# Optimization experiments

Measured on AMD Instinct MI355X. Metric: run time of the kernel, lower is better.

Reference implementation:

```python
import jax, jax.numpy as jnp
import numpy as np

HEADS, DIM_HEAD, LANDMARKS, PINV_ITERS, CONV_K = 8, 64, 256, 6, 33


def iter_pinv(x, iters=PINV_ITERS):
    # Moore-Penrose iterative pseudo-inverse (lucidrains nystrom_attention)
    abs_x = jnp.abs(x)
    scale = abs_x.sum(-1).max() * abs_x.sum(-2).max()  # global maxes, as in torch.max
    z = jnp.swapaxes(x, -1, -2) / scale
    I = jnp.eye(x.shape[-1], dtype=x.dtype)
    for _ in range(iters):
        xz = x @ z
        z = 0.25 * z @ (13.0 * I - xz @ (15.0 * I - xz @ (7.0 * I - xz)))
    return z


def nystrom_attention(h, W_qkv, W_out, b_out, conv_w):
    b, n, _ = h.shape
    inner = HEADS * DIM_HEAD
    qkv = h @ W_qkv  # (b, n, 3*inner), bias=False
    q, k, v = jnp.split(qkv, 3, axis=-1)
    split_heads = lambda t: t.reshape(b, n, HEADS, DIM_HEAD).transpose(0, 2, 1, 3)
    q, k, v = split_heads(q), split_heads(k), split_heads(v)  # (b,h,n,dh)
    q = q * (DIM_HEAD ** -0.5)
    l = n // LANDMARKS  # tokens per landmark (n divisible by m, so no padding)
    q_l = q.reshape(b, HEADS, LANDMARKS, l, DIM_HEAD).mean(3)
    k_l = k.reshape(b, HEADS, LANDMARKS, l, DIM_HEAD).mean(3)
    sim1 = jnp.einsum('bhnd,bhmd->bhnm', q, k_l)      # (b,h,n,m)
    sim2 = jnp.einsum('bhmd,bhld->bhml', q_l, k_l)    # (b,h,m,m)
    sim3 = jnp.einsum('bhmd,bhnd->bhmn', q_l, k)      # (b,h,m,n)
    attn1 = jax.nn.softmax(sim1, -1)
    attn2 = jax.nn.softmax(sim2, -1)
    attn3 = jax.nn.softmax(sim3, -1)
    out = (attn1 @ iter_pinv(attn2)) @ (attn3 @ v)    # (b,h,n,dh)
    # residual depthwise conv along sequence dim: Conv2d(heads, heads, (33,1), groups=heads, no bias)
    res = jax.lax.conv_general_dilated(
        v, conv_w, window_strides=(1, 1),
        padding=((CONV_K // 2, CONV_K // 2), (0, 0)),
        feature_group_count=HEADS)
    out = out + res
    out = out.transpose(0, 2, 1, 3).reshape(b, n, inner)
    return out @ W_out + b_out


def setup_inputs() -> dict:
    key = jax.random.key(0)
    ks = jax.random.split(key, 8)
    N, Din, Dout = 8192, 1024, 256
    inner = HEADS * DIM_HEAD
    s = 0.02
    return {
        'x': jax.random.normal(ks[0], (1, N, Din), jnp.float32),
        'W_ft': jax.random.normal(ks[1], (Din, Dout), jnp.float32) * s,
        'b_ft': jnp.zeros((Dout,), jnp.float32),
        'W_qkv': jax.random.normal(ks[2], (Dout, 3 * inner), jnp.float32) * s,
        'W_out': jax.random.normal(ks[3], (inner, Dout), jnp.float32) * s,
        'b_out': jnp.zeros((Dout,), jnp.float32),
        'conv_w': jax.random.normal(ks[4], (HEADS, 1, CONV_K, 1), jnp.float32) * s,
        'W_score': jax.random.normal(ks[5], (Dout, 1), jnp.float32) * s,
        'b_score': jnp.zeros((1,), jnp.float32),
    }


def reference(x, W_ft, b_ft, W_qkv, W_out, b_out, conv_w, W_score, b_score):
    # feature_transform: Linear -> Dropout (identity in eval) -> ReLU
    h = jax.nn.relu(x @ W_ft + b_ft)                 # (1, N, Dout)
    af = nystrom_attention(h, W_qkv, W_out, b_out, conv_w)
    # score_layer: Linear -> Dropout -> ReLU
    scores = jax.nn.relu(af @ W_score + b_score)     # (1, N, 1)
    scores = scores[0].T                             # (1, N)
    weights = jax.nn.softmax(scores, axis=1)         # (1, N)
    aggregated = weights @ h[0]                      # (1, Dout)
    return aggregated, weights
```

## Files before the change

kernel.cpp:

```cpp
#include <hip/hip_runtime.h>

typedef unsigned short u16;
typedef __attribute__((ext_vector_type(8))) short s16x8;
typedef __attribute__((ext_vector_type(4))) float f32x4;
typedef __attribute__((ext_vector_type(8))) unsigned short u16x8;

__device__ inline float b2f(u16 u) {
  unsigned x = ((unsigned)u) << 16;
  return __builtin_bit_cast(float, x);
}
__device__ inline u16 f2b(float f) {
  unsigned u = __builtin_bit_cast(unsigned, f);
  u += 0x7fffu + ((u >> 16) & 1u);
  return (u16)(u >> 16);
}

#define GLL(src, dst) __builtin_amdgcn_global_load_lds( \
    (const __attribute__((address_space(1))) unsigned int*)(src), \
    (__attribute__((address_space(3))) unsigned int*)(dst), 16, 0, 0)

struct MP {
  const u16* A; const u16* B;
  u16* C; u16* Ct; float* Cf; u16* vTo;
  const u16* Aadd; const float* bias;
  int M, N, K;
  int lda, ldb, ldc, ldct, ldcf, ldaadd;
  long long bA, bB, bC, bCt, bCf, bAadd;
  float alpha, beta;
  int relu, scale_cols; float colscale;
  int kchunks;
};

template<int BM, int BN, bool F32A>
__global__ __launch_bounds__(256) void gemm_mfma(MP p)
{
  constexpr int WM = BM / 2, WN = BN / 2;
  constexpr int FM = WM / 16, FN = WN / 16;
  constexpr int APAN = BM / 16, BPAN = BN / 16, NPAN = APAN + BPAN;
  constexpr int APW = (APAN + 3) / 4;
  __shared__ __align__(16) u16 lds[2 * NPAN * 512];

  const int tid = threadIdx.x, lane = tid & 63, wid = tid >> 6;
  const int bz = blockIdx.z;
  const int batch = (p.kchunks > 1) ? bz / p.kchunks : bz;
  const int kc    = (p.kchunks > 1) ? bz % p.kchunks : 0;
  const u16* A = p.A + (long long)batch * p.bA + (long long)kc * p.K;
  const float* Af32 = (const float*)p.A + (long long)batch * p.bA + (long long)kc * p.K;
  const u16* B = p.B + (long long)batch * p.bB + (long long)kc * p.K;
  const int m0 = blockIdx.y * BM, n0 = blockIdx.x * BN;
  const int srow = lane & 15, skoff = (lane >> 4) * 8;
  const int wm0 = (wid >> 1) * WM, wn0 = (wid & 1) * WN;

  f32x4 acc[FM][FN];
#pragma unroll
  for (int i = 0; i < FM; i++)
#pragma unroll
    for (int j = 0; j < FN; j++) acc[i][j] = (f32x4){0.f, 0.f, 0.f, 0.f};

  float4 areg[APW][2];

  auto stage_all = [&](int sb, int kt) {
#pragma unroll
    for (int pp = wid; pp < NPAN; pp += 4) {
      const u16* src = (pp < APAN)
        ? A + (size_t)(m0 + pp * 16 + srow) * p.lda + kt + skoff
        : B + (size_t)(n0 + (pp - APAN) * 16 + srow) * p.ldb + kt + skoff;
      GLL(src, &lds[sb * (NPAN * 512) + pp * 512]);
    }
  };
  auto stage_b = [&](int sb, int kt) {
#pragma unroll
    for (int pp = APAN + wid; pp < NPAN; pp += 4) {
      const u16* src = B + (size_t)(n0 + (pp - APAN) * 16 + srow) * p.ldb + kt + skoff;
      GLL(src, &lds[sb * (NPAN * 512) + pp * 512]);
    }
  };
  auto load_a = [&](int kt) {
#pragma unroll
    for (int ap = 0; ap < APW; ap++) {
      int pp = wid + ap * 4;
      const float* src = Af32 + (size_t)(m0 + pp * 16 + srow) * p.lda + kt + skoff;
      areg[ap][0] = ((const float4*)src)[0];
      areg[ap][1] = ((const float4*)src)[1];
    }
  };
  auto write_a = [&](int sb) {
#pragma unroll
    for (int ap = 0; ap < APW; ap++) {
      int pp = wid + ap * 4;
      u16 t[8];
      t[0] = f2b(areg[ap][0].x); t[1] = f2b(areg[ap][0].y);
      t[2] = f2b(areg[ap][0].z); t[3] = f2b(areg[ap][0].w);
      t[4] = f2b(areg[ap][1].x); t[5] = f2b(areg[ap][1].y);
      t[6] = f2b(areg[ap][1].z); t[7] = f2b(areg[ap][1].w);
      *(s16x8*)&lds[sb * (NPAN * 512) + pp * 512 + lane * 8] = *(const s16x8*)t;
    }
  };
  auto compute = [&](int sb) {
    const int bo = sb * (NPAN * 512);
    s16x8 afr[FM], bfr[FN];
#pragma unroll
    for (int i = 0; i < FM; i++)
      afr[i] = *(const s16x8*)&lds[bo + (wm0 / 16 + i) * 512 + lane * 8];
#pragma unroll
    for (int j = 0; j < FN; j++)
      bfr[j] = *(const s16x8*)&lds[bo + (APAN + wn0 / 16 + j) * 512 + lane * 8];
#pragma unroll
    for (int i = 0; i < FM; i++)
#pragma unroll
      for (int j = 0; j < FN; j++)
        acc[i][j] = __builtin_amdgcn_mfma_f32_16x16x32_bf16(afr[i], bfr[j], acc[i][j], 0, 0, 0);
  };

  const int nt = p.K / 32;
  int buf = 0;
  if constexpr (F32A) { load_a(0); stage_b(0, 0); write_a(0); }
  else                { stage_all(0, 0); }
  asm volatile("s_waitcnt vmcnt(0)" ::: "memory");
  __syncthreads();

  for (int t = 0; t < nt; ++t) {
    if constexpr (F32A) {
      if (t + 1 < nt) { load_a((t + 1) * 32); stage_b(buf ^ 1, (t + 1) * 32); }
      compute(buf);
      if (t + 1 < nt) write_a(buf ^ 1);
    } else {
      if (t + 1 < nt) stage_all(buf ^ 1, (t + 1) * 32);
      compute(buf);
    }
    asm volatile("s_waitcnt vmcnt(0)" ::: "memory");
    __syncthreads();
    buf ^= 1;
  }

  const int r0 = (lane >> 4) * 4, c0 = lane & 15;
#pragma unroll
  for (int i = 0; i < FM; i++) {
#pragma unroll
    for (int j = 0; j < FN; j++) {
#pragma unroll
      for (int q = 0; q < 4; q++) {
        const int gr = m0 + wm0 + i * 16 + r0 + q;
        const int gc = n0 + wn0 + j * 16 + c0;
        float c = p.alpha * acc[i][j][q];
        if (p.Aadd) c += p.beta * b2f(p.Aadd[(long long)batch * p.bAadd + (size_t)gr * p.ldaadd + gc]);
        if (p.bias) c += p.bias[gc];
        if (gc < p.scale_cols) c *= p.colscale;
        if (p.relu) c = fmaxf(c, 0.f);
        if (p.Cf) p.Cf[(long long)bz * p.bCf + (size_t)gr * p.ldcf + gc] = c;
        u16 b = f2b(c);
        if (p.C)  p.C [(long long)batch * p.bC + (size_t)gr * p.ldc + gc] = b;
        if (p.Ct) p.Ct[(long long)batch * p.bCt + (size_t)gc * p.ldct + gr] = b;
        if (p.vTo && gc >= 1024) p.vTo[(size_t)(gc - 1024) * 8192 + gr] = b;
      }
    }
  }
}

__global__ void row_stats_8192(const u16* __restrict__ S, float2* __restrict__ st)
{
  const int row = blockIdx.x, t = threadIdx.x;
  const u16x8* p8 = (const u16x8*)(S + (size_t)row * 8192);
  u16x8 r[4]; float v[32];
#pragma unroll
  for (int i = 0; i < 4; i++) r[i] = p8[i * 256 + t];
#pragma unroll
  for (int i = 0; i < 4; i++)
#pragma unroll
    for (int j = 0; j < 8; j++) v[i * 8 + j] = b2f(r[i][j]);
  float mx = -INFINITY;
#pragma unroll
  for (int i = 0; i < 32; i++) mx = fmaxf(mx, v[i]);
  __shared__ float red[256];
  red[t] = mx; __syncthreads();
  for (int s = 128; s; s >>= 1) { if (t < s) red[t] = fmaxf(red[t], red[t + s]); __syncthreads(); }
  mx = red[0]; __syncthreads();
  float ls = 0.f;
#pragma unroll
  for (int i = 0; i < 32; i++) ls += expf(v[i] - mx);
  red[t] = ls; __syncthreads();
  for (int s = 128; s; s >>= 1) { if (t < s) red[t] += red[t + s]; __syncthreads(); }
  if (t == 0) st[row] = make_float2(mx, 1.f / red[0]);
}

struct AVP { const u16* S; const float2* st; const u16* vT; float* Cf; };

__global__ __launch_bounds__(256) void av_gemm_exp(AVP p)
{
  constexpr int APAN = 8, NPAN = 12;
  __shared__ __align__(16) u16 lds[2 * NPAN * 512];
  const int tid = threadIdx.x, lane = tid & 63, wid = tid >> 6;
  const int bz = blockIdx.z, head = bz >> 4, kc = bz & 15;
  const u16* S = p.S + (size_t)head * 256 * 8192 + kc * 512;
  const u16* B = p.vT + (size_t)head * 524288 + kc * 512;
  const int m0 = blockIdx.y * 128;
  const int srow = lane & 15, skoff = (lane >> 4) * 8;
  const int wm0 = (wid >> 1) * 64, wn0 = (wid & 1) * 32;

  int rowA[2]; float am[2], ai[2];
#pragma unroll
  for (int ap = 0; ap < 2; ap++) {
    rowA[ap] = m0 + (wid + ap * 4) * 16 + srow;
    float2 s2 = p.st[head * 256 + rowA[ap]];
    am[ap] = s2.x; ai[ap] = s2.y;
  }

  f32x4 acc[4][2];
#pragma unroll
  for (int i = 0; i < 4; i++)
#pragma unroll
    for (int j = 0; j < 2; j++) acc[i][j] = (f32x4){0.f, 0.f, 0.f, 0.f};

  u16x8 areg[2];
  auto load_a = [&](int kt) {
#pragma unroll
    for (int ap = 0; ap < 2; ap++)
      areg[ap] = *(const u16x8*)(S + (size_t)rowA[ap] * 8192 + kt + skoff);
  };
  auto write_a = [&](int sb) {
#pragma unroll
    for (int ap = 0; ap < 2; ap++) {
      int pp = wid + ap * 4;
      u16 t[8];
#pragma unroll
      for (int e = 0; e < 8; e++)
        t[e] = f2b(expf(b2f(areg[ap][e]) - am[ap]) * ai[ap]);
      *(s16x8*)&lds[sb * (NPAN * 512) + pp * 512 + lane * 8] = *(const s16x8*)t;
    }
  };
  auto stage_b = [&](int sb, int kt) {
    int pp = 8 + wid;
    const u16* src = B + (size_t)((pp - 8) * 16 + srow) * 8192 + kt + skoff;
    GLL(src, &lds[sb * (NPAN * 512) + pp * 512]);
  };
  auto compute = [&](int sb) {
    const int bo = sb * (NPAN * 512);
    s16x8 afr[4], bfr[2];
#pragma unroll
    for (int i = 0; i < 4; i++)
      afr[i] = *(const s16x8*)&lds[bo + (wm0 / 16 + i) * 512 + lane * 8];
#pragma unroll
    for (int j = 0; j < 2; j++)
      bfr[j] = *(const s16x8*)&lds[bo + (APAN + wn0 / 16 + j) * 512 + lane * 8];
#pragma unroll
    for (int i = 0; i < 4; i++)
#pragma unroll
      for (int j = 0; j < 2; j++)
        acc[i][j] = __builtin_amdgcn_mfma_f32_16x16x32_bf16(afr[i], bfr[j], acc[i][j], 0, 0, 0);
  };

  const int nt = 16;
  int buf = 0;
  load_a(0); stage_b(0, 0); write_a(0);
  asm volatile("s_waitcnt vmcnt(0)" ::: "memory");
  __syncthreads();
  for (int t = 0; t < nt; ++t) {
    if (t + 1 < nt) { load_a((t + 1) * 32); stage_b(buf ^ 1, (t + 1) * 32); }
    compute(buf);
    if (t + 1 < nt) write_a(buf ^ 1);
    asm volatile("s_waitcnt vmcnt(0)" ::: "memory");
    __syncthreads();
    buf ^= 1;
  }

  const int r0 = (lane >> 4) * 4, c0 = lane & 15;
#pragma unroll
  for (int i = 0; i < 4; i++)
#pragma unroll
    for (int j = 0; j < 2; j++)
#pragma unroll
      for (int q = 0; q < 4; q++) {
        const int gr = m0 + wm0 + i * 16 + r0 + q;
        const int gc = wn0 + j * 16 + c0;
        p.Cf[(size_t)bz * 16384 + (size_t)gr * 64 + gc] = acc[i][j][q];
      }
}

struct FA1 { const u16 *qkvb, *kl, *MmT; u16 *af; };

__global__ __launch_bounds__(256) void fused_attn1(FA1 p)
{
  __shared__ __align__(16) u16 lds[36864];
  __shared__ float mb[4][64];
  const int tid = threadIdx.x, lane = tid & 63, wid = tid >> 6;
  const int head = blockIdx.y, n0 = blockIdx.x * 64;
  const int srow = lane & 15, skoff = (lane >> 4) * 8;
  const int rbase = (lane >> 4) * 4;

  for (int pid = wid; pid < 72; pid += 4) {
    const u16* src;
    if (pid < 8) {
      int pr = pid >> 1, kc = pid & 1;
      src = p.qkvb + (size_t)(n0 + pr * 16 + srow) * 1536 + head * 64 + kc * 32 + skoff;
    } else if (pid < 40) {
      int j = pid - 8, pr = j >> 1, kc = j & 1;
      src = p.kl + head * 16384 + (size_t)(pr * 16 + srow) * 64 + kc * 32 + skoff;
    } else {
      int j = pid - 40, pr = j >> 3, kc = j & 7;
      src = p.MmT + head * 16384 + (size_t)(pr * 16 + srow) * 256 + kc * 32 + skoff;
    }
    GLL(src, &lds[pid * 512]);
  }
  asm volatile("s_waitcnt vmcnt(0)" ::: "memory");
  __syncthreads();

  const int wr = (wid >> 1) * 32, ch_ = wid & 1;
  f32x4 s[2][8];
#pragma unroll
  for (int i = 0; i < 2; i++)
#pragma unroll
    for (int j = 0; j < 8; j++) s[i][j] = (f32x4){0.f, 0.f, 0.f, 0.f};
#pragma unroll
  for (int t = 0; t < 2; t++) {
    s16x8 a[2], b[8];
#pragma unroll
    for (int i = 0; i < 2; i++)
      a[i] = *(const s16x8*)&lds[(((wid >> 1) * 2 + i) * 2 + t) * 512 + lane * 8];
#pragma unroll
    for (int j = 0; j < 8; j++)
      b[j] = *(const s16x8*)&lds[4096 + ((ch_ * 8 + j) * 2 + t) * 512 + lane * 8];
#pragma unroll
    for (int i = 0; i < 2; i++)
#pragma unroll
      for (int j = 0; j < 8; j++)
        s[i][j] = __builtin_amdgcn_mfma_f32_16x16x32_bf16(a[i], b[j], s[i][j], 0, 0, 0);
  }
#pragma unroll
  for (int i = 0; i < 2; i++)
#pragma unroll
    for (int q = 0; q < 4; q++) {
      float rm = -INFINITY;
#pragma unroll
      for (int j = 0; j < 8; j++) rm = fmaxf(rm, s[i][j][q]);
#pragma unroll
      for (int off = 1; off < 16; off <<= 1) rm = fmaxf(rm, __shfl_xor(rm, off));
      if ((lane & 15) == 0) mb[ch_][wr + i * 16 + rbase + q] = rm;
    }
  __syncthreads();
  float m_[2][4];
#pragma unroll
  for (int i = 0; i < 2; i++)
#pragma unroll
    for (int q = 0; q < 4; q++)
      m_[i][q] = fmaxf(mb[0][wr + i * 16 + rbase + q], mb[1][wr + i * 16 + rbase + q]);
#pragma unroll
  for (int i = 0; i < 2; i++)
#pragma unroll
    for (int q = 0; q < 4; q++) {
      float ss = 0.f;
#pragma unroll
      for (int j = 0; j < 8; j++) {
        float e = expf(s[i][j][q] - m_[i][q]);
        s[i][j][q] = e; ss += e;
      }
#pragma unroll
      for (int off = 1; off < 16; off <<= 1) ss += __shfl_xor(ss, off);
      if ((lane & 15) == 0) mb[2 + ch_][wr + i * 16 + rbase + q] = ss;
    }
  __syncthreads();
#pragma unroll
  for (int i = 0; i < 2; i++)
#pragma unroll
    for (int q = 0; q < 4; q++) {
      int row = wr + i * 16 + rbase + q;
      float inv = 1.f / (mb[2][row] + mb[3][row]);
#pragma unroll
      for (int j = 0; j < 8; j++)
        lds[(size_t)row * 264 + ch_ * 128 + j * 16 + (lane & 15)] = f2b(s[i][j][q] * inv);
    }
  __syncthreads();
  const int wr2 = (wid >> 1) * 32, wd2 = (wid & 1) * 32;
  f32x4 acc[2][2];
#pragma unroll
  for (int i = 0; i < 2; i++)
#pragma unroll
    for (int jd = 0; jd < 2; jd++) acc[i][jd] = (f32x4){0.f, 0.f, 0.f, 0.f};
#pragma unroll
  for (int t = 0; t < 8; t++) {
    s16x8 a[2], b[2];
#pragma unroll
    for (int i = 0; i < 2; i++)
      a[i] = *(const s16x8*)&lds[(size_t)(wr2 + i * 16 + (lane & 15)) * 264 + t * 32 + (lane >> 4) * 8];
#pragma unroll
    for (int jd = 0; jd < 2; jd++)
      b[jd] = *(const s16x8*)&lds[20480 + (((wid & 1) * 2 + jd) * 8 + t) * 512 + lane * 8];
#pragma unroll
    for (int i = 0; i < 2; i++)
#pragma unroll
      for (int jd = 0; jd < 2; jd++)
        acc[i][jd] = __builtin_amdgcn_mfma_f32_16x16x32_bf16(a[i], b[jd], acc[i][jd], 0, 0, 0);
  }
#pragma unroll
  for (int i = 0; i < 2; i++)
#pragma unroll
    for (int jd = 0; jd < 2; jd++)
#pragma unroll
      for (int q = 0; q < 4; q++)
        p.af[(size_t)(n0 + wr2 + i * 16 + rbase + q) * 512 + head * 64 + wd2 + jd * 16 + (lane & 15)]
            = f2b(acc[i][jd][q]);
}

__global__ void conv_res_add_bf16(const u16* __restrict__ qkvb,
                                  const float* __restrict__ convw,
                                  u16* __restrict__ af)
{
  __shared__ float vt[96][64];
  const int h = blockIdx.y, n0 = blockIdx.x * 64;
  const int t = threadIdx.x, ch = t & 63, r0 = t >> 6;
  for (int r = r0; r < 96; r += 4) {
    int n = n0 - 16 + r;
    float v = 0.f;
    if (n >= 0 && n < 8192) v = b2f(qkvb[(size_t)n * 1536 + 1024 + h * 64 + ch]);
    vt[r][ch] = v;
  }
  __syncthreads();
  float w[33];
#pragma unroll
  for (int j = 0; j < 33; j++) w[j] = convw[h * 33 + j];
  for (int tl = r0; tl < 64; tl += 4) {
    float acc = 0.f;
#pragma unroll
    for (int j = 0; j < 33; j++) acc += w[j] * vt[tl + j][ch];
    size_t o = (size_t)(n0 + tl) * 512 + h * 64 + ch;
    af[o] = f2b(b2f(af[o]) + acc);
  }
}

__global__ void reduce_bias_bf16(const float* __restrict__ parts, int nparts,
                                 const float* __restrict__ bias, int relu,
                                 u16* __restrict__ out,
                                 const float* __restrict__ Wscore,
                                 const float* __restrict__ bscore,
                                 float* __restrict__ scores)
{
  const int i4 = blockIdx.x * 256 + threadIdx.x;
  float4 s = ((const float4*)parts)[i4];
  for (int k = 1; k < nparts; k++) {
    float4 v = ((const float4*)parts)[(size_t)k * 524288 + i4];
    s.x += v.x; s.y += v.y; s.z += v.z; s.w += v.w;
  }
  const float4 b = ((const float4*)bias)[i4 & 63];
  s.x += b.x; s.y += b.y; s.z += b.z; s.w += b.w;
  if (relu) {
    s.x = fmaxf(s.x, 0.f); s.y = fmaxf(s.y, 0.f);
    s.z = fmaxf(s.z, 0.f); s.w = fmaxf(s.w, 0.f);
  }
  if (out) {
    ushort4 o; o.x = f2b(s.x); o.y = f2b(s.y); o.z = f2b(s.z); o.w = f2b(s.w);
    ((ushort4*)out)[i4] = o;
  }
  if (Wscore) {
    const int lane = threadIdx.x & 63;
    const float4 w = ((const float4*)Wscore)[lane];
    float v = s.x * w.x + s.y * w.y + s.z * w.z + s.w * w.w;
    for (int off = 32; off; off >>= 1) v += __shfl_down(v, off);
    if (lane == 0)
      scores[blockIdx.x * 4 + (threadIdx.x >> 6)] = fmaxf(v + bscore[0], 0.f);
  }
}

__global__ void fused_tail(const float* __restrict__ scores,
                           const u16* __restrict__ hb, float* __restrict__ out)
{
  __shared__ float red[256];
  const int t = threadIdx.x, c = blockIdx.x;
  float e[32];
  float m = -INFINITY;
#pragma unroll
  for (int i = 0; i < 32; i++) { e[i] = scores[t + i * 256]; m = fmaxf(m, e[i]); }
  red[t] = m; __syncthreads();
  for (int s = 128; s; s >>= 1) { if (t < s) red[t] = fmaxf(red[t], red[t + s]); __syncthreads(); }
  m = red[0]; __syncthreads();
  float ls = 0.f;
#pragma unroll
  for (int i = 0; i < 32; i++) { e[i] = expf(e[i] - m); ls += e[i]; }
  red[t] = ls; __syncthreads();
  for (int s = 128; s; s >>= 1) { if (t < s) red[t] += red[t + s]; __syncthreads(); }
  const float inv = 1.f / red[0];
  __syncthreads();

  if (c < 256) {
    float acc = 0.f;
#pragma unroll
    for (int i = 0; i < 32; i++)
      acc += e[i] * inv * b2f(hb[(size_t)(t + i * 256) * 256 + c]);
    red[t] = acc; __syncthreads();
    for (int s = 128; s; s >>= 1) { if (t < s) red[t] += red[t + s]; __syncthreads(); }
    if (t == 0) out[c] = red[0];
  } else {
#pragma unroll
    for (int i = 0; i < 32; i++) out[256 + t + i * 256] = e[i] * inv;
  }
}

__global__ void prescale(const u16* __restrict__ x2, float* __restrict__ sbuf)
{
  const int h = blockIdx.x, t = threadIdx.x;
  const u16* X = x2 + ((size_t)h << 16);
  float cs = 0.f;
  for (int r = 0; r < 256; r++) cs += fabsf(b2f(X[r * 256 + t]));
  float rs = 0.f;
  for (int c4 = 0; c4 < 256; c4 += 4) {
    ushort4 v = *(const ushort4*)(X + (size_t)t * 256 + c4);
    rs += fabsf(b2f(v.x)) + fabsf(b2f(v.y)) + fabsf(b2f(v.z)) + fabsf(b2f(v.w));
  }
  __shared__ float red[512];
  red[t] = rs; red[256 + t] = cs;
  __syncthreads();
  for (int s = 128; s; s >>= 1) {
    if (t < s) {
      red[t] = fmaxf(red[t], red[t + s]);
      red[256 + t] = fmaxf(red[256 + t], red[256 + t + s]);
    }
    __syncthreads();
  }
  if (t == 0) { sbuf[h] = red[0]; sbuf[8 + h] = red[256]; }
}

__global__ void pinv_init(const u16* __restrict__ x2, const float* __restrict__ sbuf,
                          u16* __restrict__ z0, u16* __restrict__ z0T)
{
  __shared__ u16 tile[64][80];
  const int t = threadIdx.x;
  const size_t base = (size_t)blockIdx.y << 16;
  const int tr = (blockIdx.x >> 2) * 64, tc = (blockIdx.x & 3) * 64;
  const u16* X = x2 + base;

  float mr = -INFINITY, mc = -INFINITY;
#pragma unroll
  for (int i = 0; i < 8; i++) {
    mr = fmaxf(mr, sbuf[i]);
    mc = fmaxf(mc, sbuf[8 + i]);
  }
  const float inv = 1.f / (mr * mc);

  {
    int r = t >> 2, cg = (t & 3) * 16;
#pragma unroll
    for (int v4 = 0; v4 < 4; v4++) {
      ushort4 v = *(const ushort4*)(X + (size_t)(tr + r) * 256 + tc + cg + v4 * 4);
      v.x = f2b(b2f(v.x) * inv); v.y = f2b(b2f(v.y) * inv);
      v.z = f2b(b2f(v.z) * inv); v.w = f2b(b2f(v.w) * inv);
      *(ushort4*)(z0T + base + (size_t)(tr + r) * 256 + tc + cg + v4 * 4) = v;
      *(ushort4*)&tile[r][cg + v4 * 4] = v;
    }
  }
  __syncthreads();
  {
    int c = t >> 2, rg = (t & 3) * 16;
    u16 o[16];
#pragma unroll
    for (int e = 0; e < 16; e++) o[e] = tile[rg + e][c];
#pragma unroll
    for (int v4 = 0; v4 < 4; v4++)
      *(ushort4*)(z0 + base + (size_t)(tc + c) * 256 + tr + rg + v4 * 4) = *(ushort4*)&o[v4 * 4];
  }
}

struct PG {
  const u16 *U, *V, *Xadd, *XaddT;
  u16 *DR, *DT;
  float alpha, beta;
};

template<bool WD, bool WDT>
__global__ __launch_bounds__(256) void pinv_gemm(PG p)
{
  __shared__ __align__(16) u16 lds[65536 / 2];
  const int tid = threadIdx.x, lane = tid & 63, wid = tid >> 6;
  const size_t base = (size_t)blockIdx.z << 16;
  const u16* U = p.U + base;
  const u16* V = p.V + base;
  const int m0 = blockIdx.y * 64, n0 = blockIdx.x * 64;
  const int srow = lane & 15, skoff = (lane >> 4) * 8;
  const int wr = (wid >> 1) * 32, wc = (wid & 1) * 32;

#pragma unroll
  for (int q = 0; q < 16; q++) {
    const int pid = wid * 16 + q;
    const int rg = (pid >> 3) & 3, t = pid & 7;
    const u16* src = (pid < 32)
      ? U + (size_t)(m0 + rg * 16 + srow) * 256 + t * 32 + skoff
      : V + (size_t)(n0 + rg * 16 + srow) * 256 + t * 32 + skoff;
    GLL(src, &lds[pid * 512]);
  }
  asm volatile("s_waitcnt vmcnt(0)" ::: "memory");
  __syncthreads();

  f32x4 acc[2][2], accT[2][2];
#pragma unroll
  for (int i = 0; i < 2; i++)
#pragma unroll
    for (int j = 0; j < 2; j++) {
      acc[i][j] = (f32x4){0.f, 0.f, 0.f, 0.f};
      accT[i][j] = (f32x4){0.f, 0.f, 0.f, 0.f};
    }

#pragma unroll
  for (int t = 0; t < 8; t++) {
    s16x8 afr[2], bfr[2];
#pragma unroll
    for (int i = 0; i < 2; i++)
      afr[i] = *(const s16x8*)&lds[((wr / 16 + i) * 8 + t) * 512 + lane * 8];
#pragma unroll
    for (int j = 0; j < 2; j++)
      bfr[j] = *(const s16x8*)&lds[(32 + (wc / 16 + j) * 8 + t) * 512 + lane * 8];
#pragma unroll
    for (int i = 0; i < 2; i++)
#pragma unroll
      for (int j = 0; j < 2; j++) {
        if constexpr (WD)
          acc[i][j] = __builtin_amdgcn_mfma_f32_16x16x32_bf16(afr[i], bfr[j], acc[i][j], 0, 0, 0);
        if constexpr (WDT)
          accT[j][i] = __builtin_amdgcn_mfma_f32_16x16x32_bf16(bfr[j], afr[i], accT[j][i], 0, 0, 0);
      }
  }

  const int r0 = (lane >> 4) * 4, c0 = lane & 15;
  if constexpr (WD) {
    const u16* Xa = p.Xadd ? p.Xadd + base : nullptr;
    u16* DR = p.DR + base;
#pragma unroll
    for (int i = 0; i < 2; i++)
#pragma unroll
      for (int j = 0; j < 2; j++)
#pragma unroll
        for (int q = 0; q < 4; q++) {
          const int gr = m0 + wr + i * 16 + r0 + q;
          const int gc = n0 + wc + j * 16 + c0;
          float v = p.alpha * acc[i][j][q];
          if (Xa) v += p.beta * b2f(Xa[(size_t)gr * 256 + gc]);
          DR[(size_t)gr * 256 + gc] = f2b(v);
        }
  }
  if constexpr (WDT) {
    const u16* Xt = p.XaddT ? p.XaddT + base : nullptr;
    u16* DT = p.DT + base;
#pragma unroll
    for (int j = 0; j < 2; j++)
#pragma unroll
      for (int i = 0; i < 2; i++)
#pragma unroll
        for (int q = 0; q < 4; q++) {
          const int gn = n0 + wc + j * 16 + r0 + q;
          const int gm = m0 + wr + i * 16 + c0;
          float v = p.alpha * accT[j][i][q];
          if (Xt) v += p.beta * b2f(Xt[(size_t)gn * 256 + gm]);
          DT[(size_t)gn * 256 + gm] = f2b(v);
        }
  }
}

struct PS2 { const u16 *Am, *AmT, *zr; u16 *MT, *W, *WT; };

__global__ __launch_bounds__(256) void pinv_stage2(PS2 p)
{
  __shared__ __align__(16) u16 lds[65536 / 2];
  const int tid = threadIdx.x, lane = tid & 63, wid = tid >> 6;
  const int prob = blockIdx.z >> 3;
  const size_t base = (size_t)(blockIdx.z & 7) << 16;
  const u16* U = (prob ? p.zr : p.Am) + base;
  const u16* V = p.AmT + base;
  const int m0 = blockIdx.y * 64, n0 = blockIdx.x * 64;
  const int srow = lane & 15, skoff = (lane >> 4) * 8;
  const int wr = (wid >> 1) * 32, wc = (wid & 1) * 32;

#pragma unroll
  for (int q = 0; q < 16; q++) {
    const int pid = wid * 16 + q;
    const int rg = (pid >> 3) & 3, t = pid & 7;
    const u16* src = (pid < 32)
      ? U + (size_t)(m0 + rg * 16 + srow) * 256 + t * 32 + skoff
      : V + (size_t)(n0 + rg * 16 + srow) * 256 + t * 32 + skoff;
    GLL(src, &lds[pid * 512]);
  }
  asm volatile("s_waitcnt vmcnt(0)" ::: "memory");
  __syncthreads();

  f32x4 acc[2][2], accT[2][2];
#pragma unroll
  for (int i = 0; i < 2; i++)
#pragma unroll
    for (int j = 0; j < 2; j++) {
      acc[i][j] = (f32x4){0.f, 0.f, 0.f, 0.f};
      accT[i][j] = (f32x4){0.f, 0.f, 0.f, 0.f};
    }

#pragma unroll
  for (int t = 0; t < 8; t++) {
    s16x8 afr[2], bfr[2];
#pragma unroll
    for (int i = 0; i < 2; i++)
      afr[i] = *(const s16x8*)&lds[((wr / 16 + i) * 8 + t) * 512 + lane * 8];
#pragma unroll
    for (int j = 0; j < 2; j++)
      bfr[j] = *(const s16x8*)&lds[(32 + (wc / 16 + j) * 8 + t) * 512 + lane * 8];
#pragma unroll
    for (int i = 0; i < 2; i++)
#pragma unroll
      for (int j = 0; j < 2; j++) {
        acc[i][j]  = __builtin_amdgcn_mfma_f32_16x16x32_bf16(afr[i], bfr[j], acc[i][j], 0, 0, 0);
        accT[j][i] = __builtin_amdgcn_mfma_f32_16x16x32_bf16(bfr[j], afr[i], accT[j][i], 0, 0, 0);
      }
  }

  const int r0 = (lane >> 4) * 4, c0 = lane & 15;
  if (prob == 0) {
    const u16* At = p.AmT + base;
    u16* MT = p.MT + base;
#pragma unroll
    for (int j = 0; j < 2; j++)
#pragma unroll
      for (int i = 0; i < 2; i++)
#pragma unroll
        for (int q = 0; q < 4; q++) {
          const int gn = n0 + wc + j * 16 + r0 + q;
          const int gm = m0 + wr + i * 16 + c0;
          float v = 7.f * b2f(At[(size_t)gn * 256 + gm]) - accT[j][i][q];
          MT[(size_t)gn * 256 + gm] = f2b(v);
        }
  } else {
    u16* Wr = p.W + base;
    u16* WT = p.WT + base;
#pragma unroll
    for (int i = 0; i < 2; i++)
#pragma unroll
      for (int j = 0; j < 2; j++)
#pragma unroll
        for (int q = 0; q < 4; q++) {
          const int gr = m0 + wr + i * 16 + r0 + q;
          const int gc = n0 + wc + j * 16 + c0;
          Wr[(size_t)gr * 256 + gc] = f2b(acc[i][j][q]);
        }
#pragma unroll
    for (int j = 0; j < 2; j++)
#pragma unroll
      for (int i = 0; i < 2; i++)
#pragma unroll
        for (int q = 0; q < 4; q++) {
          const int gn = n0 + wc + j * 16 + r0 + q;
          const int gm = m0 + wr + i * 16 + c0;
          WT[(size_t)gn * 256 + gm] = f2b(accT[j][i][q]);
        }
  }
}

struct PS3 { const u16 *W, *MT, *zr, *zt, *WT; u16 *outR, *outT; };

__global__ __launch_bounds__(256) void pinv_stage3(PS3 p)
{
  __shared__ __align__(16) u16 lds[65536 / 2];
  const int tid = threadIdx.x, lane = tid & 63, wid = tid >> 6;
  const size_t base = (size_t)blockIdx.z << 16;
  const u16* U = p.W + base;
  const u16* V = p.MT + base;
  const int m0 = blockIdx.y * 64, n0 = blockIdx.x * 64;
  const int srow = lane & 15, skoff = (lane >> 4) * 8;
  const int wr = (wid >> 1) * 32, wc = (wid & 1) * 32;

#pragma unroll
  for (int q = 0; q < 16; q++) {
    const int pid = wid * 16 + q;
    const int rg = (pid >> 3) & 3, t = pid & 7;
    const u16* src = (pid < 32)
      ? U + (size_t)(m0 + rg * 16 + srow) * 256 + t * 32 + skoff
      : V + (size_t)(n0 + rg * 16 + srow) * 256 + t * 32 + skoff;
    GLL(src, &lds[pid * 512]);
  }
  asm volatile("s_waitcnt vmcnt(0)" ::: "memory");
  __syncthreads();

  f32x4 acc[2][2], accT[2][2];
#pragma unroll
  for (int i = 0; i < 2; i++)
#pragma unroll
    for (int j = 0; j < 2; j++) {
      acc[i][j] = (f32x4){0.f, 0.f, 0.f, 0.f};
      accT[i][j] = (f32x4){0.f, 0.f, 0.f, 0.f};
    }

#pragma unroll
  for (int t = 0; t < 8; t++) {
    s16x8 afr[2], bfr[2];
#pragma unroll
    for (int i = 0; i < 2; i++)
      afr[i] = *(const s16x8*)&lds[((wr / 16 + i) * 8 + t) * 512 + lane * 8];
#pragma unroll
    for (int j = 0; j < 2; j++)
      bfr[j] = *(const s16x8*)&lds[(32 + (wc / 16 + j) * 8 + t) * 512 + lane * 8];
#pragma unroll
    for (int i = 0; i < 2; i++)
#pragma unroll
      for (int j = 0; j < 2; j++) {
        acc[i][j]  = __builtin_amdgcn_mfma_f32_16x16x32_bf16(afr[i], bfr[j], acc[i][j], 0, 0, 0);
        accT[j][i] = __builtin_amdgcn_mfma_f32_16x16x32_bf16(bfr[j], afr[i], accT[j][i], 0, 0, 0);
      }
  }

  const int r0 = (lane >> 4) * 4, c0 = lane & 15;
  {
    const u16* Z = p.zr + base;
    const u16* Wm = p.W + base;
    u16* DR = p.outR + base;
#pragma unroll
    for (int i = 0; i < 2; i++)
#pragma unroll
      for (int j = 0; j < 2; j++)
#pragma unroll
        for (int q = 0; q < 4; q++) {
          const int gr = m0 + wr + i * 16 + r0 + q;
          const int gc = n0 + wc + j * 16 + c0;
          float v = 0.25f * acc[i][j][q]
                  + 3.25f * b2f(Z[(size_t)gr * 256 + gc])
                  - 3.75f * b2f(Wm[(size_t)gr * 256 + gc]);
          DR[(size_t)gr * 256 + gc] = f2b(v);
        }
  }
  {
    const u16* Zt = p.zt + base;
    const u16* Wt = p.WT + base;
    u16* DT = p.outT + base;
#pragma unroll
    for (int j = 0; j < 2; j++)
#pragma unroll
      for (int i = 0; i < 2; i++)
#pragma unroll
        for (int q = 0; q < 4; q++) {
          const int gn = n0 + wc + j * 16 + r0 + q;
          const int gm = m0 + wr + i * 16 + c0;
          float v = 0.25f * accT[j][i][q]
                  + 3.25f * b2f(Zt[(size_t)gn * 256 + gm])
                  - 3.75f * b2f(Wt[(size_t)gn * 256 + gm]);
          DT[(size_t)gn * 256 + gm] = f2b(v);
        }
  }
}

__global__ void prep_weights(const float* __restrict__ Wft, const float* __restrict__ Wqkv,
                             const float* __restrict__ Wout, u16* __restrict__ WftT,
                             u16* __restrict__ WqkvT, u16* __restrict__ WoutT)
{
  int idx = blockIdx.x * 256 + threadIdx.x;
  if (idx < 262144) {
    int r = idx & 1023, c = idx >> 10;
    WftT[idx] = f2b(Wft[(size_t)r * 256 + c]);
  } else if (idx < 655360) {
    int i = idx - 262144;
    int r = i & 255, c = i >> 8;
    WqkvT[i] = f2b(Wqkv[(size_t)r * 1536 + c]);
  } else {
    int i = idx - 655360;
    int r = i & 511, c = i >> 9;
    WoutT[i] = f2b(Wout[(size_t)r * 256 + c]);
  }
}

__global__ void landmark_means(const u16* __restrict__ qkvb,
                               u16* __restrict__ ql, u16* __restrict__ kl)
{
  int idx = blockIdx.x * 256 + threadIdx.x;
  int which = idx >> 17, r = idx & 131071;
  int h = r >> 14, m = (r >> 6) & 255, d = r & 63;
  const u16* src = qkvb + (which ? 512 : 0) + h * 64 + d;
  float s = 0.f; int n0 = m * 32;
  for (int i = 0; i < 32; i++) s += b2f(src[(size_t)(n0 + i) * 1536]);
  (which ? kl : ql)[r] = f2b(s * (1.f / 32.f));
}

__global__ void softmax_rows_bf16_256(u16* __restrict__ d)
{
  const int row = blockIdx.x * 4 + (threadIdx.x >> 6);
  const int lane = threadIdx.x & 63;
  ushort4* p = (ushort4*)(d + (size_t)row * 256);
  ushort4 raw = p[lane];
  float v0 = b2f(raw.x), v1 = b2f(raw.y), v2 = b2f(raw.z), v3 = b2f(raw.w);
  float mx = fmaxf(fmaxf(v0, v1), fmaxf(v2, v3));
  for (int off = 1; off < 64; off <<= 1) mx = fmaxf(mx, __shfl_xor(mx, off));
  v0 = expf(v0 - mx); v1 = expf(v1 - mx); v2 = expf(v2 - mx); v3 = expf(v3 - mx);
  float s = v0 + v1 + v2 + v3;
  for (int off = 1; off < 64; off <<= 1) s += __shfl_xor(s, off);
  float inv = 1.f / s;
  raw.x = f2b(v0 * inv); raw.y = f2b(v1 * inv); raw.z = f2b(v2 * inv); raw.w = f2b(v3 * inv);
  p[lane] = raw;
}

__global__ void reduce_avT(const float* __restrict__ avp, u16* __restrict__ avT)
{
  int idx = blockIdx.x * 256 + threadIdx.x;
  int m = idx & 255, d = (idx >> 8) & 63, h = idx >> 14;
  float s = 0.f;
  for (int c = 0; c < 16; c++) s += avp[((size_t)(h * 16 + c)) * 16384 + m * 64 + d];
  avT[((size_t)h * 64 + d) * 256 + m] = f2b(s);
}

extern "C" void kernel_launch(void* const* d_in, const int* in_sizes, int n_in,
                              void* d_out, int out_size, void* d_ws, size_t ws_size,
                              hipStream_t stream)
{
  const float* x       = (const float*)d_in[0];
  const float* W_ft    = (const float*)d_in[1];
  const float* b_ft    = (const float*)d_in[2];
  const float* W_qkv   = (const float*)d_in[3];
  const float* W_out   = (const float*)d_in[4];
  const float* b_out   = (const float*)d_in[5];
  const float* conv_w  = (const float*)d_in[6];
  const float* W_score = (const float*)d_in[7];
  const float* b_score = (const float*)d_in[8];
  float* out = (float*)d_out;

  char* W = (char*)d_ws;
  auto alloc = [&](size_t bytes) { char* r = W; W += (bytes + 255) & ~(size_t)255; return r; };
  u16* WftT  = (u16*)alloc(256ull * 1024 * 2);
  u16* WqkvT = (u16*)alloc(1536ull * 256 * 2);
  u16* WoutT = (u16*)alloc(256ull * 512 * 2);
  u16* hb    = (u16*)alloc(8192ull * 256 * 2);
  u16* qkvb  = (u16*)alloc(8192ull * 1536 * 2);
  u16* ql    = (u16*)alloc(8ull * 256 * 64 * 2);
  u16* kl    = (u16*)alloc(8ull * 256 * 64 * 2);
  u16* x2    = (u16*)alloc(8ull * 256 * 256 * 2);
  u16* z0    = (u16*)alloc(8ull * 256 * 256 * 2);
  u16* z0T   = (u16*)alloc(8ull * 256 * 256 * 2);
  u16* z1    = (u16*)alloc(8ull * 256 * 256 * 2);
  u16* z1T   = (u16*)alloc(8ull * 256 * 256 * 2);
  u16* Amat  = (u16*)alloc(8ull * 256 * 256 * 2);
  u16* AmatT = (u16*)alloc(8ull * 256 * 256 * 2);
  u16* T2T   = (u16*)alloc(8ull * 256 * 256 * 2);
  u16* T4T   = (u16*)alloc(8ull * 256 * 256 * 2);
  u16* Wb    = (u16*)alloc(8ull * 256 * 256 * 2);
  u16* BUF   = (u16*)alloc(8ull * 8192 * 256 * 2);
  u16* vT    = (u16*)alloc(8ull * 64 * 8192 * 2);
  float* avp = (float*)alloc(8ull * 16 * 256 * 64 * 4);
  u16* avT   = (u16*)alloc(8ull * 64 * 256 * 2);
  u16* MmT   = (u16*)alloc(8ull * 64 * 256 * 2);
  u16* af    = (u16*)alloc(8192ull * 512 * 2);
  float* gpart = (float*)alloc(4ull * 8192 * 256 * 4);
  float2* stat = (float2*)alloc(2048 * 8);
  float* sbuf   = (float*)alloc(256);
  float* scores = (float*)alloc(8192 * 4);

  auto mp = [](const u16* A, const u16* B, int M, int N, int K,
               int lda, int ldb, long long bA, long long bB) {
    MP p{}; p.A = A; p.B = B; p.M = M; p.N = N; p.K = K;
    p.lda = lda; p.ldb = ldb; p.bA = bA; p.bB = bB;
    p.alpha = 1.f; p.beta = 0.f; p.kchunks = 1; return p;
  };

  prep_weights<<<3072, 256, 0, stream>>>(W_ft, W_qkv, W_out, WftT, WqkvT, WoutT);

  { MP p = mp((const u16*)x, WftT, 8192, 256, 256, 1024, 1024, 0, 0);
    p.kchunks = 4; p.Cf = gpart; p.ldcf = 256; p.bCf = 2097152;
    gemm_mfma<64, 256, true><<<dim3(1, 128, 4), 256, 0, stream>>>(p); }
  reduce_bias_bf16<<<2048, 256, 0, stream>>>(gpart, 4, b_ft, 1, hb,
                                             nullptr, nullptr, nullptr);

  { MP p = mp(hb, WqkvT, 8192, 1536, 256, 256, 256, 0, 0);
    p.C = qkvb; p.ldc = 1536; p.scale_cols = 512; p.colscale = 0.125f; p.vTo = vT;
    gemm_mfma<128, 128, false><<<dim3(12, 64, 1), 256, 0, stream>>>(p); }

  landmark_means<<<1024, 256, 0, stream>>>(qkvb, ql, kl);

  { MP p = mp(ql, kl, 256, 256, 64, 64, 64, 16384, 16384);
    p.C = x2; p.ldc = 256; p.bC = 65536;
    gemm_mfma<64, 64, false><<<dim3(4, 4, 8), 256, 0, stream>>>(p); }
  softmax_rows_bf16_256<<<512, 256, 0, stream>>>(x2);

  prescale<<<8, 256, 0, stream>>>(x2, sbuf);
  pinv_init<<<dim3(16, 8), 256, 0, stream>>>(x2, sbuf, z0, z0T);
  {
    const dim3 g(4, 4, 8), g2(4, 4, 16), b(256);
    u16 *zr = z0, *zt = z0T, *wr_ = z1, *wt = z1T;
    for (int it = 0; it < 6; it++) {
      { PG p{x2, zt, nullptr, nullptr, Amat, AmatT, 1.f, 0.f};
        pinv_gemm<true, true><<<g, b, 0, stream>>>(p); }
      { PS2 s{Amat, AmatT, zr, T2T, Wb, T4T};
        pinv_stage2<<<g2, b, 0, stream>>>(s); }
      { PS3 s{Wb, T2T, zr, zt, T4T, wr_, wt};
        pinv_stage3<<<g, b, 0, stream>>>(s); }
      u16* t;
      t = zr; zr = wr_; wr_ = t;
      t = zt; zt = wt; wt = t;
    }
  }

  { MP p = mp(ql, qkvb + 512, 256, 8192, 64, 64, 1536, 16384, 64);
    p.C = BUF; p.ldc = 8192; p.bC = (long long)256 * 8192;
    gemm_mfma<128, 128, false><<<dim3(64, 2, 8), 256, 0, stream>>>(p); }
  row_stats_8192<<<2048, 256, 0, stream>>>(BUF, stat);

  { AVP p{BUF, stat, vT, avp};
    av_gemm_exp<<<dim3(1, 2, 128), 256, 0, stream>>>(p); }
  reduce_avT<<<512, 256, 0, stream>>>(avp, avT);

  { MP p = mp(z0, avT, 256, 64, 256, 256, 256, 65536, 16384);
    p.Ct = MmT; p.ldct = 256; p.bCt = 16384;
    gemm_mfma<64, 64, false><<<dim3(1, 4, 8), 256, 0, stream>>>(p); }

  { FA1 fp{qkvb, kl, MmT, af};
    fused_attn1<<<dim3(128, 8), 256, 0, stream>>>(fp); }

  conv_res_add_bf16<<<dim3(128, 8), 256, 0, stream>>>(qkvb, conv_w, af);

  { MP p = mp(af, WoutT, 8192, 256, 128, 512, 512, 0, 0);
    p.kchunks = 4; p.Cf = gpart; p.ldcf = 256; p.bCf = 2097152;
    gemm_mfma<64, 256, false><<<dim3(1, 128, 4), 256, 0, stream>>>(p); }
  reduce_bias_bf16<<<2048, 256, 0, stream>>>(gpart, 4, b_out, 0, nullptr,
                                             W_score, b_score, scores);

  fused_tail<<<257, 256, 0, stream>>>(scores, hb, out);
}
```

Baseline: 384.5 us.

## Restructure pinv iteration to update A=x·z recursively, two kernels per iteration

Rewrites the Newton–Schulz pseudo-inverse loop so that the product A = x·z is carried between iterations and updated with the same polynomial as z (A_new = 0.25·A·(13I − A(15I − A(7I − A)))), instead of being recomputed from x each iteration. This drops the per-iteration x·z GEMM launch, leaving two launches per iteration plus one initial x·z GEMM. The last iteration skips the A update. It also stops computing transposed outputs that are not needed, and adds more intermediate buffers. Propagating A recursively in bf16 may let rounding error build up differently from recomputing it.

New measurement: 379.1 us. No clear change (-1.4%).

```diff
diff --git a/kernel.cpp b/kernel.cpp
--- a/kernel.cpp
+++ b/kernel.cpp
@@ -651,16 +651,16 @@
   }
 }
 
-struct PS2 { const u16 *Am, *AmT, *zr; u16 *MT, *W, *WT; };
-
-__global__ __launch_bounds__(256) void pinv_stage2(PS2 p)
-{
-  __shared__ __align__(16) u16 lds[65536 / 2];
+struct PR1 { const u16 *A, *At, *z; u16 *B, *Bt, *G, *Gt, *W; };
+
+__global__ __launch_bounds__(256) void pinv_r1(PR1 p)
+{
+  __shared__ __align__(16) u16 lds[32768];
   const int tid = threadIdx.x, lane = tid & 63, wid = tid >> 6;
   const int prob = blockIdx.z >> 3;
   const size_t base = (size_t)(blockIdx.z & 7) << 16;
-  const u16* U = (prob ? p.zr : p.Am) + base;
-  const u16* V = p.AmT + base;
+  const u16* U = (prob ? p.z : p.A) + base;
+  const u16* V = p.At + base;
   const int m0 = blockIdx.y * 64, n0 = blockIdx.x * 64;
   const int srow = lane & 15, skoff = (lane >> 4) * 8;
   const int wr = (wid >> 1) * 32, wc = (wid & 1) * 32;
@@ -699,15 +699,31 @@
     for (int i = 0; i < 2; i++)
 #pragma unroll
       for (int j = 0; j < 2; j++) {
-        acc[i][j]  = __builtin_amdgcn_mfma_f32_16x16x32_bf16(afr[i], bfr[j], acc[i][j], 0, 0, 0);
-        accT[j][i] = __builtin_amdgcn_mfma_f32_16x16x32_bf16(bfr[j], afr[i], accT[j][i], 0, 0, 0);
+        acc[i][j] = __builtin_amdgcn_mfma_f32_16x16x32_bf16(afr[i], bfr[j], acc[i][j], 0, 0, 0);
+        if (prob == 0)
+          accT[j][i] = __builtin_amdgcn_mfma_f32_16x16x32_bf16(bfr[j], afr[i], accT[j][i], 0, 0, 0);
       }
   }
 
   const int r0 = (lane >> 4) * 4, c0 = lane & 15;
   if (prob == 0) {
-    const u16* At = p.AmT + base;
-    u16* MT = p.MT + base;
+    const u16* Ab  = p.A  + base;
+    const u16* Atb = p.At + base;
+    u16 *Bv = p.B + base, *Btv = p.Bt + base;
+    u16 *Gv = p.G + base, *Gtv = p.Gt + base;
+#pragma unroll
+    for (int i = 0; i < 2; i++)
+#pragma unroll
+      for (int j = 0; j < 2; j++)
+#pragma unroll
+        for (int q = 0; q < 4; q++) {
+          const int gr = m0 + wr + i * 16 + r0 + q;
+          const int gc = n0 + wc + j * 16 + c0;
+          float b = acc[i][j][q];
+          float a = b2f(Ab[(size_t)gr * 256 + gc]);
+          Bv[(size_t)gr * 256 + gc] = f2b(b);
+          Gv[(size_t)gr * 256 + gc] = f2b(7.f * a - b);
+        }
 #pragma unroll
     for (int j = 0; j < 2; j++)
 #pragma unroll
@@ -716,12 +732,13 @@
         for (int q = 0; q < 4; q++) {
           const int gn = n0 + wc + j * 16 + r0 + q;
           const int gm = m0 + wr + i * 16 + c0;
-          float v = 7.f * b2f(At[(size_t)gn * 256 + gm]) - accT[j][i][q];
-          MT[(size_t)gn * 256 + gm] = f2b(v);
+          float bt = accT[j][i][q];
+          float at = b2f(Atb[(size_t)gn * 256 + gm]);
+          Btv[(size_t)gn * 256 + gm] = f2b(bt);
+          Gtv[(size_t)gn * 256 + gm] = f2b(7.f * at - bt);
         }
   } else {
-    u16* Wr = p.W + base;
-    u16* WT = p.WT + base;
+    u16* Wv = p.W + base;
 #pragma unroll
     for (int i = 0; i < 2; i++)
 #pragma unroll
@@ -730,30 +747,21 @@
         for (int q = 0; q < 4; q++) {
           const int gr = m0 + wr + i * 16 + r0 + q;
           const int gc = n0 + wc + j * 16 + c0;
-          Wr[(size_t)gr * 256 + gc] = f2b(acc[i][j][q]);
+          Wv[(size_t)gr * 256 + gc] = f2b(acc[i][j][q]);
         }
-#pragma unroll
-    for (int j = 0; j < 2; j++)
-#pragma unroll
-      for (int i = 0; i < 2; i++)
-#pragma unroll
-        for (int q = 0; q < 4; q++) {
-          const int gn = n0 + wc + j * 16 + r0 + q;
-          const int gm = m0 + wr + i * 16 + c0;
-          WT[(size_t)gn * 256 + gm] = f2b(accT[j][i][q]);
-        }
-  }
-}
-
-struct PS3 { const u16 *W, *MT, *zr, *zt, *WT; u16 *outR, *outT; };
-
-__global__ __launch_bounds__(256) void pinv_stage3(PS3 p)
-{
-  __shared__ __align__(16) u16 lds[65536 / 2];
+  }
+}
+
+struct PR2 { const u16 *W, *G, *Gt, *B, *Bt, *z, *A, *At; u16 *zo, *Ao, *Aot; };
+
+__global__ __launch_bounds__(256) void pinv_r2(PR2 p)
+{
+  __shared__ __align__(16) u16 lds[32768];
   const int tid = threadIdx.x, lane = tid & 63, wid = tid >> 6;
-  const size_t base = (size_t)blockIdx.z << 16;
-  const u16* U = p.W + base;
-  const u16* V = p.MT + base;
+  const int prob = blockIdx.z >> 3;
+  const size_t base = (size_t)(blockIdx.z & 7) << 16;
+  const u16* U = (prob ? p.G  : p.W ) + base;
+  const u16* V = (prob ? p.Bt : p.Gt) + base;
   const int m0 = blockIdx.y * 64, n0 = blockIdx.x * 64;
   const int srow = lane & 15, skoff = (lane >> 4) * 8;
   const int wr = (wid >> 1) * 32, wc = (wid & 1) * 32;
@@ -792,16 +800,17 @@
     for (int i = 0; i < 2; i++)
 #pragma unroll
       for (int j = 0; j < 2; j++) {
-        acc[i][j]  = __builtin_amdgcn_mfma_f32_16x16x32_bf16(afr[i], bfr[j], acc[i][j], 0, 0, 0);
-        accT[j][i] = __builtin_amdgcn_mfma_f32_16x16x32_bf16(bfr[j], afr[i], accT[j][i], 0, 0, 0);
+        acc[i][j] = __builtin_amdgcn_mfma_f32_16x16x32_bf16(afr[i], bfr[j], acc[i][j], 0, 0, 0);
+        if (prob)
+          accT[j][i] = __builtin_amdgcn_mfma_f32_16x16x32_bf16(bfr[j], afr[i], accT[j][i], 0, 0, 0);
       }
   }
 
   const int r0 = (lane >> 4) * 4, c0 = lane & 15;
-  {
-    const u16* Z = p.zr + base;
-    const u16* Wm = p.W + base;
-    u16* DR = p.outR + base;
+  if (prob == 0) {
+    const u16* Zb = p.z + base;
+    const u16* Wb = p.W + base;
+    u16* Zo = p.zo + base;
 #pragma unroll
     for (int i = 0; i < 2; i++)
 #pragma unroll
@@ -811,15 +820,30 @@
           const int gr = m0 + wr + i * 16 + r0 + q;
           const int gc = n0 + wc + j * 16 + c0;
           float v = 0.25f * acc[i][j][q]
-                  + 3.25f * b2f(Z[(size_t)gr * 256 + gc])
-                  - 3.75f * b2f(Wm[(size_t)gr * 256 + gc]);
-          DR[(size_t)gr * 256 + gc] = f2b(v);
+                  + 3.25f * b2f(Zb[(size_t)gr * 256 + gc])
+                  - 3.75f * b2f(Wb[(size_t)gr * 256 + gc]);
+          Zo[(size_t)gr * 256 + gc] = f2b(v);
         }
-  }
-  {
-    const u16* Zt = p.zt + base;
-    const u16* Wt = p.WT + base;
-    u16* DT = p.outT + base;
+  } else {
+    const u16* Ab  = p.A  + base;
+    const u16* Bb  = p.B  + base;
+    const u16* Atb = p.At + base;
+    const u16* Btb = p.Bt + base;
+    u16* Ao  = p.Ao  + base;
+    u16* Aot = p.Aot + base;
+#pragma unroll
+    for (int i = 0; i < 2; i++)
+#pragma unroll
+      for (int j = 0; j < 2; j++)
+#pragma unroll
+        for (int q = 0; q < 4; q++) {
+          const int gr = m0 + wr + i * 16 + r0 + q;
+          const int gc = n0 + wc + j * 16 + c0;
+          float v = 0.25f * acc[i][j][q]
+                  + 3.25f * b2f(Ab[(size_t)gr * 256 + gc])
+                  - 3.75f * b2f(Bb[(size_t)gr * 256 + gc]);
+          Ao[(size_t)gr * 256 + gc] = f2b(v);
+        }
 #pragma unroll
     for (int j = 0; j < 2; j++)
 #pragma unroll
@@ -829,9 +853,9 @@
           const int gn = n0 + wc + j * 16 + r0 + q;
           const int gm = m0 + wr + i * 16 + c0;
           float v = 0.25f * accT[j][i][q]
-                  + 3.25f * b2f(Zt[(size_t)gn * 256 + gm])
-                  - 3.75f * b2f(Wt[(size_t)gn * 256 + gm]);
-          DT[(size_t)gn * 256 + gm] = f2b(v);
+                  + 3.25f * b2f(Atb[(size_t)gn * 256 + gm])
+                  - 3.75f * b2f(Btb[(size_t)gn * 256 + gm]);
+          Aot[(size_t)gn * 256 + gm] = f2b(v);
         }
   }
 }
@@ -920,13 +944,16 @@
   u16* x2    = (u16*)alloc(8ull * 256 * 256 * 2);
   u16* z0    = (u16*)alloc(8ull * 256 * 256 * 2);
   u16* z0T   = (u16*)alloc(8ull * 256 * 256 * 2);
-  u16* z1    = (u16*)alloc(8ull * 256 * 256 * 2);
-  u16* z1T   = (u16*)alloc(8ull * 256 * 256 * 2);
+  u16* zp    = (u16*)alloc(8ull * 256 * 256 * 2);
   u16* Amat  = (u16*)alloc(8ull * 256 * 256 * 2);
   u16* AmatT = (u16*)alloc(8ull * 256 * 256 * 2);
-  u16* T2T   = (u16*)alloc(8ull * 256 * 256 * 2);
-  u16* T4T   = (u16*)alloc(8ull * 256 * 256 * 2);
-  u16* Wb    = (u16*)alloc(8ull * 256 * 256 * 2);
+  u16* Am2   = (u16*)alloc(8ull * 256 * 256 * 2);
+  u16* Am2T  = (u16*)alloc(8ull * 256 * 256 * 2);
+  u16* Bm    = (u16*)alloc(8ull * 256 * 256 * 2);
+  u16* BmT   = (u16*)alloc(8ull * 256 * 256 * 2);
+  u16* Gm    = (u16*)alloc(8ull * 256 * 256 * 2);
+  u16* GmT   = (u16*)alloc(8ull * 256 * 256 * 2);
+  u16* Wm    = (u16*)alloc(8ull * 256 * 256 * 2);
   u16* BUF   = (u16*)alloc(8ull * 8192 * 256 * 2);
   u16* vT    = (u16*)alloc(8ull * 64 * 8192 * 2);
   float* avp = (float*)alloc(8ull * 16 * 256 * 64 * 4);
@@ -966,19 +993,21 @@
 
   prescale<<<8, 256, 0, stream>>>(x2, sbuf);
   pinv_init<<<dim3(16, 8), 256, 0, stream>>>(x2, sbuf, z0, z0T);
+  { PG p{x2, z0T, nullptr, nullptr, Amat, AmatT, 1.f, 0.f};
+    pinv_gemm<true, true><<<dim3(4, 4, 8), 256, 0, stream>>>(p); }
   {
-    const dim3 g(4, 4, 8), g2(4, 4, 16), b(256);
-    u16 *zr = z0, *zt = z0T, *wr_ = z1, *wt = z1T;
+    const dim3 b(256);
+    u16 *zr = z0, *zo = zp;
+    u16 *Ar = Amat, *Art = AmatT, *Ao = Am2, *Aot = Am2T;
     for (int it = 0; it < 6; it++) {
-      { PG p{x2, zt, nullptr, nullptr, Amat, AmatT, 1.f, 0.f};
-        pinv_gemm<true, true><<<g, b, 0, stream>>>(p); }
-      { PS2 s{Amat, AmatT, zr, T2T, Wb, T4T};
-        pinv_stage2<<<g2, b, 0, stream>>>(s); }
-      { PS3 s{Wb, T2T, zr, zt, T4T, wr_, wt};
-        pinv_stage3<<<g, b, 0, stream>>>(s); }
+      { PR1 r{Ar, Art, zr, Bm, BmT, Gm, GmT, Wm};
+        pinv_r1<<<dim3(4, 4, 16), b, 0, stream>>>(r); }
+      { PR2 r{Wm, Gm, GmT, Bm, BmT, zr, Ar, Art, zo, Ao, Aot};
+        pinv_r2<<<dim3(4, 4, (it == 5) ? 8 : 16), b, 0, stream>>>(r); }
       u16* t;
-      t = zr; zr = wr_; wr_ = t;
-      t = zt; zt = wt; wt = t;
+      t = zr; zr = zo; zo = t;
+      t = Ar; Ar = Ao; Ao = t;
+      t = Art; Art = Aot; Aot = t;
     }
   }
 
```
